# Optimization experiments

Hardware: AMD Instinct MI355X
Metric: run time of the kernel (lower is better)

## Reference

```python
import jax, jax.numpy as jnp
import numpy as np

B, L, C, H, W = 4, 16, 64, 64, 64
F, NH, NB = 128, 2, 2


def _ln(x, w, b, eps=1e-5):
    # LayerNorm over last two dims (H, W), torch-style biased variance
    m = jnp.mean(x, axis=(-2, -1), keepdims=True)
    v = jnp.var(x, axis=(-2, -1), keepdims=True)
    return (x - m) * jax.lax.rsqrt(v + eps) * w + b


def _conv2d(x, w, b):
    # x: (N, Cin, H, W), w: (Cout, Cin, k, k) -- the (1,k,k) Conv3d acts per-frame
    y = jax.lax.conv_general_dilated(x, w, (1, 1), 'SAME',
                                     dimension_numbers=('NCHW', 'OIHW', 'NCHW'))
    return y + b[None, :, None, None]


def _combine(c1, c2):
    a1, b1 = c1
    a2, b2 = c2
    return a1 * a2, a2 * b1 + b2


def _forward(x, params_log, pBw_r, pBw_i, pBb_r, pBb_i, pCw_r, pCw_i, pCb_r, pCb_i,
             lru_ln_w, lru_ln_b, cin_w, cin_b, h3_w, h3_b, h1_w, h1_b,
             h_ln_w, h_ln_b, cout_w, cout_b, ffn_ln_w, ffn_ln_b):
    gelu = lambda t: jax.nn.gelu(t, approximate=False)
    Bsz, Ln, Cc, Hh, Ww = x.shape
    for i in range(NB):
        # ---- ConvLRULayer ----
        pl = params_log[i]
        nu = jnp.exp(pl[:Cc])            # (C, H)
        theta = jnp.exp(pl[Cc:2 * Cc])   # (C, H)
        gamma = jnp.exp(pl[2 * Cc:])     # (C, H)
        lamb = jnp.exp(jax.lax.complex(-nu, theta))  # (C, H) complex
        Bw = jax.lax.complex(pBw_r[i], pBw_i[i])
        Bb = jax.lax.complex(pBb_r[i], pBb_i[i])
        Cw = jax.lax.complex(pCw_r[i], pCw_i[i])
        Cb = jax.lax.complex(pCb_r[i], pCb_i[i])
        h = jnp.fft.fft2(x.astype(jnp.complex64), axes=(-2, -1))  # (B,L,C,H,W)
        h = jnp.einsum('blchw,oc->blohw', h, Bw) + Bb[None, None, :, None, None]
        h = h * gamma[None, None, :, :, None]
        # parallel scan: h[t] = lamb * h[t-1] + h[t] along L
        a = jnp.broadcast_to(lamb[None, None, :, :, None], (Bsz, Ln, Cc, Hh, 1))
        _, h = jax.lax.associative_scan(_combine, (a, h), axis=1)
        h = jnp.fft.ifft2(h, axes=(-2, -1))
        h = jnp.einsum('blchw,oc->blohw', h, Cw) + Cb[None, None, :, None, None]
        h = _ln(h.real, lru_ln_w[i], lru_ln_b[i])
        x = h + x
        # ---- FeedForward (all Conv3d have kernel 1 in L -> per-frame 2D) ----
        y = x.reshape(Bsz * Ln, Cc, Hh, Ww)
        y_ = gelu(_conv2d(y, cin_w[i], cin_b[i]))  # (B*L, F, H, W)
        for j in range(NH):
            t = gelu(_conv2d(y_, h3_w[i, j], h3_b[i, j]))
            t = gelu(jnp.einsum('nfhw,of->nohw', t, h1_w[i, j])
                     + h1_b[i, j][None, :, None, None])
            y_ = _ln(t, h_ln_w[i, j], h_ln_b[i, j]) + y_
        t = jnp.einsum('nfhw,of->nohw', y_, cout_w[i]) + cout_b[i][None, :, None, None]
        t = _ln(t, ffn_ln_w[i], ffn_ln_b[i])
        x = t.reshape(Bsz, Ln, Cc, Hh, Ww) + x
    return x


def setup_inputs() -> dict:
    key = jax.random.key(0)
    ks = jax.random.split(key, 16)
    x = jax.random.normal(ks[0], (B, L, C, H, W), jnp.float32)
    # LRU stability init (as in the torch module)
    r_min, r_max = 0.8, 0.99
    u1 = jax.random.uniform(ks[1], (NB, C, H), jnp.float32)
    u2 = jax.random.uniform(ks[2], (NB, C, H), jnp.float32)
    nu_log = jnp.log(-0.5 * jnp.log(u1 * (r_max ** 2 - r_min ** 2) + r_min ** 2))
    theta_log = jnp.log(u2 * 2.0 * np.pi)
    gamma_log = 0.5 * jnp.log(1.0 - jnp.exp(-2.0 * jnp.exp(nu_log)))
    params_log = jnp.concatenate([nu_log, theta_log, gamma_log], axis=1)  # (NB, 3C, H)

    def nrm(k, shape, fan_in):
        return jax.random.normal(k, shape, jnp.float32) / np.sqrt(fan_in)

    return dict(
        x=x, params_log=params_log,
        pBw_r=nrm(ks[3], (NB, C, C), C), pBw_i=jnp.zeros((NB, C, C), jnp.float32),
        pBb_r=jnp.zeros((NB, C), jnp.float32), pBb_i=jnp.zeros((NB, C), jnp.float32),
        pCw_r=nrm(ks[4], (NB, C, C), C), pCw_i=jnp.zeros((NB, C, C), jnp.float32),
        pCb_r=jnp.zeros((NB, C), jnp.float32), pCb_i=jnp.zeros((NB, C), jnp.float32),
        lru_ln_w=jnp.ones((NB, H, W), jnp.float32), lru_ln_b=jnp.zeros((NB, H, W), jnp.float32),
        cin_w=nrm(ks[5], (NB, F, C, 7, 7), C * 49), cin_b=jnp.zeros((NB, F), jnp.float32),
        h3_w=nrm(ks[6], (NB, NH, F, F, 3, 3), F * 9), h3_b=jnp.zeros((NB, NH, F), jnp.float32),
        h1_w=nrm(ks[7], (NB, NH, F, F), F), h1_b=jnp.zeros((NB, NH, F), jnp.float32),
        h_ln_w=jnp.ones((NB, NH, H, W), jnp.float32), h_ln_b=jnp.zeros((NB, NH, H, W), jnp.float32),
        cout_w=nrm(ks[8], (NB, C, F), F), cout_b=jnp.zeros((NB, C), jnp.float32),
        ffn_ln_w=jnp.ones((NB, H, W), jnp.float32), ffn_ln_b=jnp.zeros((NB, H, W), jnp.float32),
    )


def reference(x, params_log, pBw_r, pBw_i, pBb_r, pBb_i, pCw_r, pCw_i, pCb_r, pCb_i,
              lru_ln_w, lru_ln_b, cin_w, cin_b, h3_w, h3_b, h1_w, h1_b,
              h_ln_w, h_ln_b, cout_w, cout_b, ffn_ln_w, ffn_ln_b):
    return _forward(x, params_log, pBw_r, pBw_i, pBb_r, pBb_i, pCw_r, pCw_i,
                    pCb_r, pCb_i, lru_ln_w, lru_ln_b, cin_w, cin_b, h3_w, h3_b,
                    h1_w, h1_b, h_ln_w, h_ln_b, cout_w, cout_b, ffn_ln_w, ffn_ln_b)
```

## Files before the change

### kernel.cpp

```cpp
#include <hip/hip_runtime.h>
#include <math.h>

static constexpr int Bd = 4, Ld = 16, Cd = 64, Hd = 64, Wd = 64, Fd = 128;
static constexpr int NBLK = 2, NHEAD = 2;
static constexpr int HW = 4096;
static constexpr float TWO_PI = 6.28318530717958647692f;

typedef __attribute__((ext_vector_type(8))) short bf16x8;
typedef __attribute__((ext_vector_type(4))) float f32x4;
typedef __attribute__((ext_vector_type(4))) unsigned int u32x4;

__device__ __forceinline__ float gelu_f(float v) {
    float x2 = v * v;
    float u = v * (0.797884560802865f + 0.0356774081363f * x2);
    float au = fabsf(u);
    float e = __expf(-2.f * au);
    float th = (1.f - e) * __builtin_amdgcn_rcpf(1.f + e);
    th = copysignf(th, u);
    return 0.5f * v * (1.f + th);
}

__device__ __forceinline__ unsigned short bf16c(float f) {
    unsigned int u = __float_as_uint(f);
    unsigned int r = (u + 0x7fffu + ((u >> 16) & 1u)) >> 16;
    return (unsigned short)r;
}
__device__ __forceinline__ float bf2f(unsigned short u) {
    return __uint_as_float((unsigned int)u << 16);
}
__device__ __forceinline__ unsigned int packbf(float r, float i) {
    return (unsigned int)bf16c(r) | ((unsigned int)bf16c(i) << 16);
}
__device__ __forceinline__ bf16x8 bneg(bf16x8 v) {
    u32x4 u = *(u32x4*)&v;
    u = u ^ 0x80008000u;
    return *(bf16x8*)&u;
}

__device__ __forceinline__ void gl2lds16(const void* g, void* l) {
    __builtin_amdgcn_global_load_lds(
        (const __attribute__((address_space(1))) void*)g,
        (__attribute__((address_space(3))) void*)l, 16, 0, 0);
}

__global__ void k_prepdft(unsigned short* __restrict__ o) {
    int idx = blockIdx.x * 256 + threadIdx.x;
    if (idx >= 16384) return;
    int sec = idx >> 12, j = idx & 4095;
    int a = j >> 6, b = j & 63;
    float ang = (TWO_PI / 64.f) * (float)((a * b) & 63);
    float sv, cv;
    __sincosf(ang, &sv, &cv);
    float v;
    if (sec == 0) v = cv;
    else if (sec == 1) v = -sv;
    else if (sec == 2) v = cv * (1.f / 64.f);
    else v = -sv * (1.f / 64.f);
    o[idx] = bf16c(v);
}

__global__ void k_preplru(const float* __restrict__ bwr, const float* __restrict__ bwi,
                          const float* __restrict__ cwr, const float* __restrict__ cwi,
                          const float* __restrict__ gl,
                          unsigned short* __restrict__ wout, float* __restrict__ gamT) {
    int idx = blockIdx.x * 256 + threadIdx.x;
    if (idx < 16384) {
        int sec = idx >> 12, j = idx & 4095;
        const float* s = (sec == 0) ? bwr : (sec == 1) ? bwi : (sec == 2) ? cwr : cwi;
        wout[idx] = bf16c(s[j]);
    } else if (idx < 20480) {
        int j = idx - 16384;
        int fh = j >> 6, o2 = j & 63;
        gamT[j] = __expf(gl[o2 * 64 + fh]);
    }
}

__global__ __launch_bounds__(256) void k_dfthm(const float* __restrict__ x,
                                               unsigned int* __restrict__ X,
                                               const unsigned short* __restrict__ tcb,
                                               const unsigned short* __restrict__ tsb) {
    __shared__ __align__(16) unsigned char smm[49152];
    unsigned char* xpT = smm;
    unsigned char* tC = smm + 32768;
    unsigned char* tS = smm + 40960;
    int blk = blockIdx.x;
    int fi = blk >> 4;
    int w0 = (blk & 15) * 4;
    int t = threadIdx.x, lane = t & 63, wv = t >> 6;
    int pl = lane & 15, kg = lane >> 4;
    int l3 = lane >> 3, l7 = lane & 7;

    for (int q = 0; q < 2; ++q) {
        int sg = q * 4 + wv;
        gl2lds16(tcb + (size_t)(sg * 8 + l3) * 64 + (l7 ^ l3) * 8, tC + sg * 1024);
        gl2lds16(tsb + (size_t)(sg * 8 + l3) * 64 + (l7 ^ l3) * 8, tS + sg * 1024);
    }
    const float* xf = x + (size_t)fi * Cd * HW;
    int h = t & 63;
    for (int k = 0; k < 16; ++k) {
        int c = k * 4 + (t >> 6);
        float4 v = *(const float4*)(xf + (size_t)c * HW + h * 64 + w0);
        float vv[4] = {v.x, v.y, v.z, v.w};
#pragma unroll
        for (int q = 0; q < 4; ++q) {
            int pos = q * 64 + c;
            *(unsigned short*)(xpT + pos * 128 + ((h * 2) ^ ((c & 7) << 4))) = bf16c(vv[q]);
        }
    }
    __syncthreads();

    int w = w0 + wv;
    unsigned int* Xw = X + (size_t)fi * 262144 + (size_t)w * 4096;
    for (int half = 0; half < 2; ++half) {
        f32x4 aR[2][4], aI[2][4];
#pragma unroll
        for (int mt = 0; mt < 2; ++mt)
#pragma unroll
            for (int nt = 0; nt < 4; ++nt) { aR[mt][nt] = (f32x4)0.f; aI[mt][nt] = (f32x4)0.f; }
#pragma unroll
        for (int ks = 0; ks < 2; ++ks) {
            int koff = (ks * 64 + kg * 16);
            bf16x8 ac[2], as_[2], b[4];
#pragma unroll
            for (int mt = 0; mt < 2; ++mt) {
                int row = half * 32 + mt * 16 + pl;
                int off = row * 128 + (koff ^ ((pl & 7) << 4));
                ac[mt] = *(const bf16x8*)(tC + off);
                as_[mt] = *(const bf16x8*)(tS + off);
            }
#pragma unroll
            for (int nt = 0; nt < 4; ++nt) {
                int pos = wv * 64 + nt * 16 + pl;
                b[nt] = *(const bf16x8*)(xpT + pos * 128 + (koff ^ ((pl & 7) << 4)));
            }
#pragma unroll
            for (int mt = 0; mt < 2; ++mt)
#pragma unroll
                for (int nt = 0; nt < 4; ++nt) {
                    aR[mt][nt] = __builtin_amdgcn_mfma_f32_16x16x32_bf16(ac[mt], b[nt], aR[mt][nt], 0, 0, 0);
                    aI[mt][nt] = __builtin_amdgcn_mfma_f32_16x16x32_bf16(as_[mt], b[nt], aI[mt][nt], 0, 0, 0);
                }
        }
#pragma unroll
        for (int mt = 0; mt < 2; ++mt)
#pragma unroll
            for (int nt = 0; nt < 4; ++nt) {
                int c = nt * 16 + pl;
#pragma unroll
                for (int r = 0; r < 4; ++r) {
                    int fh = half * 32 + mt * 16 + kg * 4 + r;
                    Xw[fh * 64 + c] = packbf(aR[mt][nt][r], aI[mt][nt][r]);
                }
            }
    }
}

__global__ __launch_bounds__(256) void k_lrumid(unsigned int* __restrict__ X,
                                                const unsigned short* __restrict__ wbr,
                                                const unsigned short* __restrict__ wbi,
                                                const unsigned short* __restrict__ wcr,
                                                const unsigned short* __restrict__ wci,
                                                const float* __restrict__ gamT,
                                                const float* __restrict__ br_g,
                                                const float* __restrict__ bi_g,
                                                const float* __restrict__ plg) {
    __shared__ __align__(16) unsigned char smm[81920];
    unsigned char* inr = smm;
    unsigned char* ini = smm + 8192;
    unsigned char* hre = smm + 16384;
    unsigned char* him = smm + 24576;
    unsigned char* wBR = smm + 32768;
    unsigned char* wBI = smm + 40960;
    unsigned char* wCR = smm + 49152;
    unsigned char* wCI = smm + 57344;
    float* gam = (float*)(smm + 65536);
    int blk = blockIdx.x;
    int b = blk >> 6, s = blk & 63;
    int t = threadIdx.x, lane = t & 63, wv = t >> 6;
    int pj = lane & 15, kg = lane >> 4;
    int l3 = lane >> 3, l7 = lane & 7;

    for (int q = 0; q < 2; ++q) {
        int sg = q * 4 + wv;
        size_t goff = (size_t)(sg * 8 + l3) * 64 + (l7 ^ l3) * 8;
        gl2lds16(wbr + goff, wBR + sg * 1024);
        gl2lds16(wbi + goff, wBI + sg * 1024);
        gl2lds16(wcr + goff, wCR + sg * 1024);
        gl2lds16(wci + goff, wCI + sg * 1024);
    }
    for (int j = t; j < 4096; j += 256) gam[j] = gamT[j];

    float lamr[4][4], lami[4][4];
#pragma unroll
    for (int nt = 0; nt < 4; ++nt) {
        int o = nt * 16 + pj;
#pragma unroll
        for (int r = 0; r < 4; ++r) {
            int fh = wv * 16 + kg * 4 + r;
            float nu = expf(plg[o * 64 + fh]);
            float th = expf(plg[4096 + o * 64 + fh]);
            float mag = expf(-nu);
            float sth, cth;
            sincosf(th, &sth, &cth);
            lamr[nt][r] = mag * cth;
            lami[nt][r] = mag * sth;
        }
    }
    float bRo[4], bIo[4];
#pragma unroll
    for (int nt = 0; nt < 4; ++nt) {
        bRo[nt] = (s == 0) ? br_g[nt * 16 + pj] : 0.f;
        bIo[nt] = (s == 0) ? bi_g[nt * 16 + pj] : 0.f;
    }
    float str[4][4], sti[4][4];
    unsigned int* Xfrm = X + (size_t)b * 16 * 262144 + (size_t)s * 4096;

    for (int l = 0; l < 16; ++l) {
        unsigned int* Xi = Xfrm + (size_t)l * 262144;
        __syncthreads();
        for (int k = 0; k < 4; ++k) {
            int j = k * 256 + t;
            int row = j >> 4, c0 = (j & 15) * 4;
            u32x4 v = *(const u32x4*)(Xi + (size_t)row * 64 + c0);
            unsigned int rw0 = (v.x & 0xffffu) | (v.y << 16);
            unsigned int rw1 = (v.z & 0xffffu) | (v.w << 16);
            unsigned int iw0 = (v.x >> 16) | (v.y & 0xffff0000u);
            unsigned int iw1 = (v.z >> 16) | (v.w & 0xffff0000u);
            int off = row * 128 + ((((c0 >> 3) ^ (row & 7)) << 4) | ((c0 & 7) * 2));
            *(unsigned int*)(inr + off) = rw0;
            *(unsigned int*)(inr + off + 4) = rw1;
            *(unsigned int*)(ini + off) = iw0;
            *(unsigned int*)(ini + off + 4) = iw1;
        }
        __syncthreads();

        f32x4 cR[4], cI[4];
#pragma unroll
        for (int nt = 0; nt < 4; ++nt) { cR[nt] = (f32x4)0.f; cI[nt] = (f32x4)0.f; }
#pragma unroll
        for (int ks = 0; ks < 2; ++ks) {
            int koff = ks * 64 + kg * 16;
            int aoff = (wv * 16 + pj) * 128 + (koff ^ ((pj & 7) << 4));
            bf16x8 ar = *(const bf16x8*)(inr + aoff);
            bf16x8 ai = *(const bf16x8*)(ini + aoff);
            bf16x8 an = bneg(ai);
#pragma unroll
            for (int nt = 0; nt < 4; ++nt) {
                int o = nt * 16 + pj;
                int woff = o * 128 + (koff ^ ((pj & 7) << 4));
                bf16x8 brf = *(const bf16x8*)(wBR + woff);
                bf16x8 bif = *(const bf16x8*)(wBI + woff);
                cR[nt] = __builtin_amdgcn_mfma_f32_16x16x32_bf16(ar, brf, cR[nt], 0, 0, 0);
                cR[nt] = __builtin_amdgcn_mfma_f32_16x16x32_bf16(an, bif, cR[nt], 0, 0, 0);
                cI[nt] = __builtin_amdgcn_mfma_f32_16x16x32_bf16(ar, bif, cI[nt], 0, 0, 0);
                cI[nt] = __builtin_amdgcn_mfma_f32_16x16x32_bf16(ai, brf, cI[nt], 0, 0, 0);
            }
        }
#pragma unroll
        for (int nt = 0; nt < 4; ++nt) {
            int o = nt * 16 + pj;
#pragma unroll
            for (int r = 0; r < 4; ++r) {
                int row = wv * 16 + kg * 4 + r;
                float g = gam[row * 64 + o];
                float vr = (cR[nt][r] + bRo[nt]) * g;
                float vi = (cI[nt][r] + bIo[nt]) * g;
                if (l == 0) {
                    str[nt][r] = vr;
                    sti[nt][r] = vi;
                } else {
                    float nr = lamr[nt][r] * str[nt][r] - lami[nt][r] * sti[nt][r] + vr;
                    float ni = lamr[nt][r] * sti[nt][r] + lami[nt][r] * str[nt][r] + vi;
                    str[nt][r] = nr;
                    sti[nt][r] = ni;
                }
                int hoff = row * 128 + ((((o >> 3) ^ (row & 7)) << 4) | ((o & 7) * 2));
                *(unsigned short*)(hre + hoff) = bf16c(str[nt][r]);
                *(unsigned short*)(him + hoff) = bf16c(sti[nt][r]);
            }
        }
        __syncthreads();

        f32x4 dR[4], dI[4];
#pragma unroll
        for (int nt = 0; nt < 4; ++nt) { dR[nt] = (f32x4)0.f; dI[nt] = (f32x4)0.f; }
#pragma unroll
        for (int ks = 0; ks < 2; ++ks) {
            int koff = ks * 64 + kg * 16;
            int aoff = (wv * 16 + pj) * 128 + (koff ^ ((pj & 7) << 4));
            bf16x8 ar = *(const bf16x8*)(hre + aoff);
            bf16x8 ai = *(const bf16x8*)(him + aoff);
            bf16x8 an = bneg(ai);
#pragma unroll
            for (int nt = 0; nt < 4; ++nt) {
                int o = nt * 16 + pj;
                int woff = o * 128 + (koff ^ ((pj & 7) << 4));
                bf16x8 brf = *(const bf16x8*)(wCR + woff);
                bf16x8 bif = *(const bf16x8*)(wCI + woff);
                dR[nt] = __builtin_amdgcn_mfma_f32_16x16x32_bf16(ar, brf, dR[nt], 0, 0, 0);
                dR[nt] = __builtin_amdgcn_mfma_f32_16x16x32_bf16(an, bif, dR[nt], 0, 0, 0);
                dI[nt] = __builtin_amdgcn_mfma_f32_16x16x32_bf16(ar, bif, dI[nt], 0, 0, 0);
                dI[nt] = __builtin_amdgcn_mfma_f32_16x16x32_bf16(ai, brf, dI[nt], 0, 0, 0);
            }
        }
#pragma unroll
        for (int nt = 0; nt < 4; ++nt) {
            int o = nt * 16 + pj;
#pragma unroll
            for (int r = 0; r < 4; ++r) {
                int row = wv * 16 + kg * 4 + r;
                Xi[(size_t)row * 64 + o] = packbf(dR[nt][r], dI[nt][r]);
            }
        }
    }
}

__global__ __launch_bounds__(256) void k_idfthm_ln(const unsigned int* __restrict__ X,
                                                   const unsigned short* __restrict__ tic,
                                                   const unsigned short* __restrict__ tis,
                                                   const float* __restrict__ cbr,
                                                   const float* __restrict__ lnw,
                                                   const float* __restrict__ lnb,
                                                   const float* __restrict__ xprev,
                                                   float* __restrict__ xout) {
    __shared__ __align__(16) unsigned char smm[81920];
    unsigned char* SrT = smm;
    unsigned char* SiT = smm + 32768;
    unsigned char* tC = smm + 65536;
    unsigned char* tS = smm + 73728;
    float* y4 = (float*)smm;
    int blk = blockIdx.x;
    int fi = blk >> 4;
    int c0 = (blk & 15) * 4;
    int t = threadIdx.x, lane = t & 63, wv = t >> 6;
    int pl = lane & 15, kg = lane >> 4;
    int l3 = lane >> 3, l7 = lane & 7;

    for (int q = 0; q < 2; ++q) {
        int sg = q * 4 + wv;
        gl2lds16(tic + (size_t)(sg * 8 + l3) * 64 + (l7 ^ l3) * 8, tC + sg * 1024);
        gl2lds16(tis + (size_t)(sg * 8 + l3) * 64 + (l7 ^ l3) * 8, tS + sg * 1024);
    }
    const unsigned int* Xf = X + (size_t)fi * 262144;
    int fh = t & 63;
    for (int k = 0; k < 16; ++k) {
        int w = k * 4 + (t >> 6);
        u32x4 v = *(const u32x4*)(Xf + (size_t)w * 4096 + fh * 64 + c0);
        unsigned int vv[4] = {v.x, v.y, v.z, v.w};
#pragma unroll
        for (int cj = 0; cj < 4; ++cj) {
            int pos2 = w * 4 + cj;
            int off = pos2 * 128 + ((fh * 2) ^ ((pos2 & 7) << 4));
            *(unsigned short*)(SrT + off) = (unsigned short)(vv[cj] & 0xffffu);
            *(unsigned short*)(SiT + off) = (unsigned short)(vv[cj] >> 16);
        }
    }
    __syncthreads();

    f32x4 y[4][4];
#pragma unroll
    for (int mt = 0; mt < 4; ++mt)
#pragma unroll
        for (int nt = 0; nt < 4; ++nt) y[mt][nt] = (f32x4)0.f;
#pragma unroll
    for (int ks = 0; ks < 2; ++ks) {
        int koff = ks * 64 + kg * 16;
        bf16x8 ac[4], as_[4], brf[4], bif[4];
#pragma unroll
        for (int mt = 0; mt < 4; ++mt) {
            int row = mt * 16 + pl;
            int off = row * 128 + (koff ^ ((pl & 7) << 4));
            ac[mt] = *(const bf16x8*)(tC + off);
            as_[mt] = *(const bf16x8*)(tS + off);
        }
#pragma unroll
        for (int nt = 0; nt < 4; ++nt) {
            int pos2 = wv * 64 + nt * 16 + pl;
            int off = pos2 * 128 + (koff ^ ((pl & 7) << 4));
            brf[nt] = *(const bf16x8*)(SrT + off);
            bif[nt] = *(const bf16x8*)(SiT + off);
        }
#pragma unroll
        for (int mt = 0; mt < 4; ++mt)
#pragma unroll
            for (int nt = 0; nt < 4; ++nt) {
                y[mt][nt] = __builtin_amdgcn_mfma_f32_16x16x32_bf16(ac[mt], brf[nt], y[mt][nt], 0, 0, 0);
                y[mt][nt] = __builtin_amdgcn_mfma_f32_16x16x32_bf16(as_[mt], bif[nt], y[mt][nt], 0, 0, 0);
            }
    }
    __syncthreads();

    float cb4[4];
#pragma unroll
    for (int cj = 0; cj < 4; ++cj) cb4[cj] = cbr[c0 + cj];
#pragma unroll
    for (int mt = 0; mt < 4; ++mt)
#pragma unroll
        for (int nt = 0; nt < 4; ++nt) {
            int pos2 = wv * 64 + nt * 16 + pl;
            int w = pos2 >> 2, cj = pos2 & 3;
#pragma unroll
            for (int r = 0; r < 4; ++r) {
                int h = mt * 16 + kg * 4 + r;
                y4[cj * 4232 + h * 66 + w] = y[mt][nt][r] + cb4[cj];
            }
        }
    __syncthreads();

    int w = lane;
    const float* yp = y4 + wv * 4232;
    float s = 0.f, q = 0.f;
    for (int h = 0; h < 64; ++h) {
        float v = yp[h * 66 + w];
        s += v;
        q += v * v;
    }
#pragma unroll
    for (int off = 32; off; off >>= 1) {
        s += __shfl_xor(s, off);
        q += __shfl_xor(q, off);
    }
    float m = s * (1.f / 4096.f);
    float var = q * (1.f / 4096.f) - m * m;
    float rs = rsqrtf(var + 1e-5f);
    int c = c0 + wv;
    const float* xp = xprev + ((size_t)fi * Cd + c) * HW;
    float* xo = xout + ((size_t)fi * Cd + c) * HW;
    for (int h = 0; h < 64; ++h) {
        int p = h * 64 + w;
        xo[p] = (yp[h * 66 + w] - m) * rs * lnw[p] + lnb[p] + xp[p];
    }
}

__global__ __launch_bounds__(256) void k_ln_res(const unsigned short* __restrict__ t_in,
                                                const float* __restrict__ w,
                                                const float* __restrict__ b,
                                                float* __restrict__ dst) {
    __shared__ float red[8];
    int fr = blockIdx.x;
    int t = threadIdx.x;
    const unsigned short* src = t_in + (size_t)fr * HW + t * 16;
    float* d = dst + (size_t)fr * HW + t * 16;
    u32x4 v0 = *(const u32x4*)(src);
    u32x4 v1 = *(const u32x4*)(src + 8);
    float vals[16];
    unsigned int vw[8] = {v0.x, v0.y, v0.z, v0.w, v1.x, v1.y, v1.z, v1.w};
#pragma unroll
    for (int j = 0; j < 8; ++j) {
        vals[j * 2] = bf2f((unsigned short)(vw[j] & 0xffffu));
        vals[j * 2 + 1] = bf2f((unsigned short)(vw[j] >> 16));
    }
    float s = 0.f, sq = 0.f;
#pragma unroll
    for (int j = 0; j < 16; ++j) { s += vals[j]; sq += vals[j] * vals[j]; }
    for (int off = 32; off; off >>= 1) {
        s += __shfl_down(s, off);
        sq += __shfl_down(sq, off);
    }
    int wid = t >> 6;
    if ((t & 63) == 0) { red[wid] = s; red[4 + wid] = sq; }
    __syncthreads();
    s = red[0] + red[1] + red[2] + red[3];
    sq = red[4] + red[5] + red[6] + red[7];
    float m = s * (1.f / 4096.f);
    float var = sq * (1.f / 4096.f) - m * m;
    float rs = rsqrtf(var + 1e-5f);
    const float* wp = w + t * 16;
    const float* bp = b + t * 16;
#pragma unroll
    for (int q4 = 0; q4 < 4; ++q4) {
        float4 wv4 = *(const float4*)(wp + q4 * 4);
        float4 bv4 = *(const float4*)(bp + q4 * 4);
        float4 dv = *(const float4*)(d + q4 * 4);
        dv.x += (vals[q4 * 4 + 0] - m) * rs * wv4.x + bv4.x;
        dv.y += (vals[q4 * 4 + 1] - m) * rs * wv4.y + bv4.y;
        dv.z += (vals[q4 * 4 + 2] - m) * rs * wv4.z + bv4.z;
        dv.w += (vals[q4 * 4 + 3] - m) * rs * wv4.w + bv4.w;
        *(float4*)(d + q4 * 4) = dv;
    }
}

__global__ void k_prep7(const float* __restrict__ w, unsigned short* __restrict__ o) {
    int idx = blockIdx.x * 256 + threadIdx.x;
    if (idx < 49 * 128 * 64) {
        int tap = idx >> 13, rem = idx & 8191, f = rem >> 6, c = rem & 63;
        o[idx] = bf16c(w[(size_t)(f * 64 + c) * 49 + tap]);
    }
}
__global__ void k_prep3(const float* __restrict__ w, unsigned short* __restrict__ o,
                        int nh) {
    int idx = blockIdx.x * 256 + threadIdx.x;
    if (idx < nh * 147456) {
        int head = idx / 147456;
        int rem = idx - head * 147456;
        int tap = rem >> 14, r2 = rem & 16383, f = r2 >> 7, c = r2 & 127;
        o[idx] = bf16c(w[(size_t)head * 147456 + (size_t)(f * 128 + c) * 9 + tap]);
    }
}
__global__ void k_prepcvt(const float* __restrict__ w, unsigned short* __restrict__ o, int n) {
    int idx = blockIdx.x * 256 + threadIdx.x;
    if (idx < n) o[idx] = bf16c(w[idx]);
}

__global__ __launch_bounds__(256) void k_t2p(const float* __restrict__ x,
                                             unsigned short* __restrict__ xT) {
    __shared__ float tile[64][65];
    int blk = blockIdx.x;
    int f = blk >> 6;
    int p0 = (blk & 63) * 64;
    int t = threadIdx.x;
    const float* src = x + (size_t)f * Cd * HW;
    for (int j = t; j < 4096; j += 256) {
        int c = j >> 6, p = j & 63;
        tile[c][p] = src[(size_t)c * HW + p0 + p];
    }
    __syncthreads();
    unsigned short* dst = xT + ((size_t)f * HW + p0) * 64;
    for (int j = t; j < 4096; j += 256) {
        int p = j >> 6, c = j & 63;
        dst[(size_t)p * 64 + c] = bf16c(tile[c][p]);
    }
}

__global__ __launch_bounds__(512) void k_conv7m(const unsigned short* __restrict__ xT,
                                                const unsigned short* __restrict__ wb,
                                                const float* __restrict__ bias,
                                                unsigned short* __restrict__ yout) {
    __shared__ __align__(16) unsigned char smm[158208];
    unsigned char* inT = smm;
    unsigned char* wt0 = smm + 125440;
    int blk = blockIdx.x;
    int fi = blk >> 3;
    int y0 = (blk & 7) * 8;
    int t = threadIdx.x, lane = t & 63, wv = t >> 6;
    int l3 = lane >> 3, l7 = lane & 7;

    const unsigned short* xf = xT + (size_t)fi * HW * 64;
    float4 z4 = make_float4(0.f, 0.f, 0.f, 0.f);
    int ksw_in = l7 ^ ((3 + l3) & 7);
    for (int idx = wv; idx < 112; idx += 8) {
        int r = idx >> 3, sg = idx & 7;
        int srow = y0 + r - 3;
        unsigned char* dst = inT + r * 8960 + 3 * 128 + sg * 1024;
        if (srow >= 0 && srow < 64) {
            gl2lds16(xf + (size_t)srow * 4096 + (sg * 8 + l3) * 64 + ksw_in * 8, dst);
        } else {
            *(float4*)(dst + lane * 16) = z4;
        }
    }
    for (int j = t; j < 672; j += 512) {
        int r = j / 48, k = j % 48;
        int xp = (k < 24) ? (k >> 3) : 67 + ((k - 24) >> 3);
        *(float4*)(inT + r * 8960 + xp * 128 + (k & 7) * 16) = z4;
    }
    int ksw_w = l7 ^ l3;
    for (int q = 0; q < 2; ++q) {
        int sg = q * 8 + wv;
        int f = sg * 8 + l3;
        gl2lds16(wb + (size_t)f * 64 + ksw_w * 8, wt0 + sg * 1024);
    }
    __syncthreads();

    int wm = wv & 3, wn = wv >> 2;
    f32x4 acc[8][4];
#pragma unroll
    for (int m = 0; m < 8; ++m)
#pragma unroll
        for (int n = 0; n < 4; ++n) acc[m][n] = (f32x4)0.f;
    int kg = lane >> 4, pl = lane & 15;
    int cur = 0;
    for (int tap = 0; tap < 49; ++tap) {
        if (tap + 1 < 49) {
            const unsigned short* g = wb + (size_t)(tap + 1) * 8192;
            unsigned char* wdst = wt0 + (cur ^ 1) * 16384;
            for (int q = 0; q < 2; ++q) {
                int sg = q * 8 + wv;
                int f = sg * 8 + l3;
                gl2lds16(g + (size_t)f * 64 + ksw_w * 8, wdst + sg * 1024);
            }
        }
        unsigned char* wcur = wt0 + cur * 16384;
        int ky = tap / 7, kx = tap % 7;
#pragma unroll
        for (int ks = 0; ks < 2; ++ks) {
            bf16x8 a[8], b[4];
#pragma unroll
            for (int m = 0; m < 8; ++m) {
                int row = wm * 2 + (m >> 2) + ky;
                int xp = (m & 3) * 16 + pl + kx;
                a[m] = *(const bf16x8*)(inT + row * 8960 + xp * 128 +
                                        (((ks * 4 + kg) ^ (xp & 7)) << 4));
            }
#pragma unroll
            for (int n = 0; n < 4; ++n) {
                int rowf = wn * 64 + n * 16 + pl;
                b[n] = *(const bf16x8*)(wcur + rowf * 128 +
                                        (((ks * 4 + kg) ^ (pl & 7)) << 4));
            }
#pragma unroll
            for (int m = 0; m < 8; ++m)
#pragma unroll
                for (int n = 0; n < 4; ++n)
                    acc[m][n] = __builtin_amdgcn_mfma_f32_16x16x32_bf16(a[m], b[n], acc[m][n], 0, 0, 0);
        }
        __syncthreads();
        cur ^= 1;
    }
    unsigned short* yo = yout + ((size_t)fi * HW + (size_t)y0 * 64) * 128;
#pragma unroll
    for (int m = 0; m < 8; ++m) {
        int rowl = wm * 2 + (m >> 2);
#pragma unroll
        for (int n = 0; n < 4; ++n) {
            int f = wn * 64 + n * 16 + pl;
            float bs = bias[f];
#pragma unroll
            for (int r = 0; r < 4; ++r) {
                int x = (m & 3) * 16 + kg * 4 + r;
                yo[(size_t)(rowl * 64 + x) * 128 + f] = bf16c(gelu_f(acc[m][n][r] + bs));
            }
        }
    }
}

__global__ __launch_bounds__(512) void k_conv3f(const unsigned short* __restrict__ yin,
                                                const unsigned short* __restrict__ wb,
                                                const float* __restrict__ bias3,
                                                const unsigned short* __restrict__ w1,
                                                const float* __restrict__ bias1,
                                                unsigned short* __restrict__ outp2,
                                                float* __restrict__ lnpart) {
    __shared__ __align__(16) unsigned char smm[163840];
    unsigned char* inT = smm;
    unsigned char* wt0 = smm + 98304;
    int blk = blockIdx.x;
    int fi = blk >> 4;
    int y0 = (blk & 15) * 4;
    int t = threadIdx.x, lane = t & 63, wv = t >> 6;
    int l4 = lane >> 4, l15 = lane & 15;
    const unsigned short* yf = yin + (size_t)fi * HW * 128;
    float4 z4 = make_float4(0.f, 0.f, 0.f, 0.f);
    for (int seg = wv; seg < 96; seg += 8) {
        int r = seg >> 4, xs = seg & 15;
        int srow = y0 + r - 1;
        int col = xs * 4 + l4;
        unsigned char* dst = inT + r * 16384 + xs * 4 * 256;
        if (srow >= 0 && srow < 64) {
            int gs = l15 ^ (col & 7);
            gl2lds16(yf + ((size_t)(srow * 64 + col) * 128 + gs * 8), dst);
        } else {
            *(float4*)(dst + lane * 16) = z4;
        }
    }
    for (int q = 0; q < 4; ++q) {
        int sg = q * 8 + wv;
        int f = sg * 4 + l4;
        gl2lds16(wb + (size_t)f * 128 + (l15 ^ (f & 7)) * 8, wt0 + sg * 1024);
    }
    __syncthreads();

    int wm = wv & 3, wn = wv >> 2;
    f32x4 acc[4][4];
#pragma unroll
    for (int m = 0; m < 4; ++m)
#pragma unroll
        for (int n = 0; n < 4; ++n) acc[m][n] = (f32x4)0.f;
    int kg = lane >> 4, pl = lane & 15;
    bf16x8 z8 = (bf16x8)(short)0;
    int cur = 0;
#pragma unroll
    for (int tap = 0; tap < 9; ++tap) {
        if (tap + 1 < 9) {
            const unsigned short* g = wb + (size_t)(tap + 1) * 16384;
            unsigned char* wdst = wt0 + (cur ^ 1) * 32768;
            for (int q = 0; q < 4; ++q) {
                int sg = q * 8 + wv;
                int f = sg * 4 + l4;
                gl2lds16(g + (size_t)f * 128 + (l15 ^ (f & 7)) * 8, wdst + sg * 1024);
            }
        }
        unsigned char* wcur = wt0 + cur * 32768;
        const int ky = tap / 3, kx = tap % 3;
        int rbase = (wm + ky) * 16384;
#pragma unroll
        for (int ks = 0; ks < 4; ++ks) {
            bf16x8 a[4], b[4];
#pragma unroll
            for (int m = 0; m < 4; ++m) {
                int col = m * 16 + pl + kx - 1;
                int colc = col;
                if (kx == 0 && m == 0) colc = (col < 0) ? 0 : col;
                if (kx == 2 && m == 3) colc = (col > 63) ? 63 : col;
                a[m] = *(const bf16x8*)(inT + rbase + colc * 256 +
                                        ((ks * 64 + kg * 16) ^ ((colc & 7) << 4)));
                if (kx == 0 && m == 0) a[m] = (pl == 0) ? z8 : a[m];
                if (kx == 2 && m == 3) a[m] = (pl == 15) ? z8 : a[m];
            }
#pragma unroll
            for (int n = 0; n < 4; ++n) {
                int row = wn * 64 + n * 16 + pl;
                b[n] = *(const bf16x8*)(wcur + (size_t)row * 256 +
                                        ((ks * 64 + kg * 16) ^ ((pl & 7) << 4)));
            }
#pragma unroll
            for (int m = 0; m < 4; ++m)
#pragma unroll
                for (int n = 0; n < 4; ++n)
                    acc[m][n] = __builtin_amdgcn_mfma_f32_16x16x32_bf16(a[m], b[n], acc[m][n], 0, 0, 0);
        }
        __syncthreads();
        cur ^= 1;
    }

    unsigned char* tL = smm;
    unsigned char* w1L = smm + 65536;
    float (*redS)[64] = (float (*)[64])(smm + 155648);
    float (*redQ)[64] = (float (*)[64])(smm + 157696);
#pragma unroll
    for (int m = 0; m < 4; ++m)
#pragma unroll
        for (int n = 0; n < 4; ++n) {
            int f = wn * 64 + n * 16 + pl;
            float bs = bias3[f];
#pragma unroll
            for (int r = 0; r < 4; ++r) {
                int pos = wm * 64 + m * 16 + kg * 4 + r;
                *(unsigned short*)(tL + (size_t)pos * 256 +
                    ((((f >> 3) ^ (pos & 7)) << 4) | ((f & 7) * 2))) =
                    bf16c(gelu_f(acc[m][n][r] + bs));
            }
        }
    for (int sg = wv; sg < 32; sg += 8) {
        int rr = sg * 4 + l4;
        gl2lds16(w1 + (size_t)rr * 128 + (l15 ^ (rr & 7)) * 8, w1L + sg * 1024);
    }
    __syncthreads();

    f32x4 fa[4][4];
#pragma unroll
    for (int m = 0; m < 4; ++m)
#pragma unroll
        for (int n = 0; n < 4; ++n) fa[m][n] = (f32x4)0.f;
#pragma unroll
    for (int ks = 0; ks < 4; ++ks) {
        bf16x8 a[4], b[4];
#pragma unroll
        for (int m = 0; m < 4; ++m) {
            int row = wm * 64 + m * 16 + pl;
            a[m] = *(const bf16x8*)(tL + (size_t)row * 256 +
                                    ((ks * 64 + kg * 16) ^ ((pl & 7) << 4)));
        }
#pragma unroll
        for (int n = 0; n < 4; ++n) {
            int row = wn * 64 + n * 16 + pl;
            b[n] = *(const bf16x8*)(w1L + (size_t)row * 256 +
                                    ((ks * 64 + kg * 16) ^ ((pl & 7) << 4)));
        }
#pragma unroll
        for (int m = 0; m < 4; ++m)
#pragma unroll
            for (int n = 0; n < 4; ++n)
                fa[m][n] = __builtin_amdgcn_mfma_f32_16x16x32_bf16(a[m], b[n], fa[m][n], 0, 0, 0);
    }
    __syncthreads();

    int slab = blk & 15;
    int p0 = slab * 256;
    unsigned char* oL = smm;
#pragma unroll
    for (int n = 0; n < 4; ++n) {
        int f = wn * 64 + n * 16 + pl;
        float bs = bias1[f];
        float s = 0.f, q = 0.f;
#pragma unroll
        for (int m = 0; m < 4; ++m)
#pragma unroll
            for (int r = 0; r < 4; ++r) {
                float v = gelu_f(fa[m][n][r] + bs);
                int pos = wm * 64 + m * 16 + kg * 4 + r;
                *(unsigned short*)(oL + (size_t)pos * 256 +
                    ((((f >> 3) ^ (pos & 7)) << 4) | ((f & 7) * 2))) = bf16c(v);
                s += v;
                q += v * v;
            }
        s += __shfl_xor(s, 16); s += __shfl_xor(s, 32);
        q += __shfl_xor(q, 16); q += __shfl_xor(q, 32);
        if (kg == 0) { redS[wv][n * 16 + pl] = s; redQ[wv][n * 16 + pl] = q; }
    }
    __syncthreads();
    unsigned char* o0 = (unsigned char*)(outp2 + ((size_t)fi * HW + p0) * 128);
#pragma unroll
    for (int it = 0; it < 8; ++it) {
        int gid = it * 512 + t;
        int pos = gid >> 4, g = gid & 15;
        u32x4 v = *(const u32x4*)(oL + (size_t)pos * 256 + ((g ^ (pos & 7)) << 4));
        *(u32x4*)(o0 + (size_t)pos * 256 + g * 16) = v;
    }
    if (t < 128) {
        int wh = t >> 6, j = t & 63;
        float s = redS[wh * 4][j] + redS[wh * 4 + 1][j] + redS[wh * 4 + 2][j] + redS[wh * 4 + 3][j];
        float q = redQ[wh * 4][j] + redQ[wh * 4 + 1][j] + redQ[wh * 4 + 2][j] + redQ[wh * 4 + 3][j];
        float* lp = lnpart + ((size_t)(fi * 16 + slab) * 128 + t) * 2;
        lp[0] = s;
        lp[1] = q;
    }
}

__global__ __launch_bounds__(256) void k_lnapply2(const unsigned short* __restrict__ t2,
                                                  const float* __restrict__ lnpart,
                                                  const float* __restrict__ w,
                                                  const float* __restrict__ b,
                                                  unsigned short* __restrict__ y) {
    __shared__ float sm_m[128], sm_r[128];
    int blk = blockIdx.x;
    int fi = blk >> 5, p0 = (blk & 31) * 128;
    int t = threadIdx.x;
    if (t < 128) {
        float s = 0.f, q = 0.f;
        for (int sl = 0; sl < 16; ++sl) {
            const float* lp = lnpart + ((size_t)(fi * 16 + sl) * 128 + t) * 2;
            s += lp[0];
            q += lp[1];
        }
        float m = s * (1.f / 4096.f);
        float var = q * (1.f / 4096.f) - m * m;
        sm_m[t] = m;
        sm_r[t] = rsqrtf(var + 1e-5f);
    }
    __syncthreads();
    int f0 = (t & 15) * 8, prow = t >> 4;
    float mm[8], rr[8];
#pragma unroll
    for (int j = 0; j < 8; ++j) { mm[j] = sm_m[f0 + j]; rr[j] = sm_r[f0 + j]; }
#pragma unroll
    for (int pass = 0; pass < 8; ++pass) {
        int p = p0 + pass * 16 + prow;
        size_t idx = ((size_t)fi * HW + p) * 128 + f0;
        u32x4 tv = *(const u32x4*)(t2 + idx);
        u32x4 yv = *(const u32x4*)(y + idx);
        float wp = w[p], bp = b[p];
        unsigned int tw[4] = {tv.x, tv.y, tv.z, tv.w};
        unsigned int yw[4] = {yv.x, yv.y, yv.z, yv.w};
        unsigned int ow[4];
#pragma unroll
        for (int q4 = 0; q4 < 4; ++q4) {
            float t0 = bf2f((unsigned short)(tw[q4] & 0xffffu));
            float t1 = bf2f((unsigned short)(tw[q4] >> 16));
            float y0 = bf2f((unsigned short)(yw[q4] & 0xffffu));
            float y1 = bf2f((unsigned short)(yw[q4] >> 16));
            float o0 = y0 + (t0 - mm[q4 * 2]) * rr[q4 * 2] * wp + bp;
            float o1 = y1 + (t1 - mm[q4 * 2 + 1]) * rr[q4 * 2 + 1] * wp + bp;
            ow[q4] = packbf(o0, o1);
        }
        u32x4 ov;
        ov.x = ow[0]; ov.y = ow[1]; ov.z = ow[2]; ov.w = ow[3];
        *(u32x4*)(y + idx) = ov;
    }
}

__global__ __launch_bounds__(256) void k_coutm(const unsigned short* __restrict__ yin,
                                               const unsigned short* __restrict__ wt,
                                               const float* __restrict__ bias,
                                               unsigned short* __restrict__ outp) {
    __shared__ __align__(16) unsigned char smm[49152];
    unsigned char* inL = smm;
    unsigned char* wL = smm + 32768;
    int blk = blockIdx.x;
    int fi = blk >> 5;
    int p0 = (blk & 31) * 128;
    int t = threadIdx.x, lane = t & 63, wv = t >> 6;
    int l4 = lane >> 4, l15 = lane & 15;
    for (int sg = wv; sg < 16; sg += 4) {
        int r = sg * 4 + l4;
        gl2lds16(wt + (size_t)r * 128 + (l15 ^ (r & 7)) * 8, wL + sg * 1024);
    }
    const unsigned short* yb = yin + (size_t)fi * HW * 128;
    for (int sg = wv; sg < 32; sg += 4) {
        int pos = sg * 4 + l4;
        gl2lds16(yb + ((size_t)(p0 + pos) * 128 + (l15 ^ (pos & 7)) * 8), inL + sg * 1024);
    }
    __syncthreads();
    int wm = wv & 1, wn = wv >> 1;
    f32x4 acc[2][4];
#pragma unroll
    for (int m = 0; m < 2; ++m)
#pragma unroll
        for (int n = 0; n < 4; ++n) acc[m][n] = (f32x4)0.f;
    int kg = lane >> 4, pl = lane & 15;
#pragma unroll
    for (int ks = 0; ks < 4; ++ks) {
        bf16x8 a[2], b[4];
#pragma unroll
        for (int m = 0; m < 2; ++m) {
            int row = wm * 32 + m * 16 + pl;
            a[m] = *(const bf16x8*)(wL + (size_t)row * 256 +
                                    ((ks * 64 + kg * 16) ^ ((pl & 7) << 4)));
        }
#pragma unroll
        for (int n = 0; n < 4; ++n) {
            int row = wn * 64 + n * 16 + pl;
            b[n] = *(const bf16x8*)(inL + (size_t)row * 256 +
                                    ((ks * 64 + kg * 16) ^ ((pl & 7) << 4)));
        }
#pragma unroll
        for (int m = 0; m < 2; ++m)
#pragma unroll
            for (int n = 0; n < 4; ++n)
                acc[m][n] = __builtin_amdgcn_mfma_f32_16x16x32_bf16(a[m], b[n], acc[m][n], 0, 0, 0);
    }
    __syncthreads();
    unsigned char* oL = smm;
#pragma unroll
    for (int m = 0; m < 2; ++m)
#pragma unroll
        for (int n = 0; n < 4; ++n) {
            int posl = wn * 64 + n * 16 + pl;
#pragma unroll
            for (int r = 0; r < 4; ++r) {
                int c = wm * 32 + m * 16 + kg * 4 + r;
                *(unsigned short*)(oL + (size_t)c * 256 +
                    ((((posl >> 3) ^ (c & 7)) << 4) | ((posl & 7) * 2))) =
                    bf16c(acc[m][n][r] + bias[c]);
            }
        }
    __syncthreads();
#pragma unroll
    for (int it = 0; it < 4; ++it) {
        int gid = it * 256 + t;
        int c = gid >> 4, g = gid & 15;
        u32x4 v = *(const u32x4*)(oL + (size_t)c * 256 + ((g ^ (c & 7)) << 4));
        *(u32x4*)((unsigned char*)(outp + ((size_t)fi * 64 + c) * HW + p0) + g * 16) = v;
    }
}

extern "C" void kernel_launch(void* const* d_in, const int* in_sizes, int n_in,
                              void* d_out, int out_size, void* d_ws, size_t ws_size,
                              hipStream_t stream) {
    (void)in_sizes; (void)n_in; (void)out_size;
    const float* x_in  = (const float*)d_in[0];
    const float* pl    = (const float*)d_in[1];
    const float* pBw_r = (const float*)d_in[2];
    const float* pBw_i = (const float*)d_in[3];
    const float* pBb_r = (const float*)d_in[4];
    const float* pBb_i = (const float*)d_in[5];
    const float* pCw_r = (const float*)d_in[6];
    const float* pCw_i = (const float*)d_in[7];
    const float* pCb_r = (const float*)d_in[8];
    const float* pCb_i = (const float*)d_in[9];
    const float* lruw  = (const float*)d_in[10];
    const float* lrub  = (const float*)d_in[11];
    const float* cinw  = (const float*)d_in[12];
    const float* cinb  = (const float*)d_in[13];
    const float* h3w   = (const float*)d_in[14];
    const float* h3b   = (const float*)d_in[15];
    const float* h1w   = (const float*)d_in[16];
    const float* h1b   = (const float*)d_in[17];
    const float* hlnw  = (const float*)d_in[18];
    const float* hlnb  = (const float*)d_in[19];
    const float* coutw = (const float*)d_in[20];
    const float* coutb = (const float*)d_in[21];
    const float* flnw  = (const float*)d_in[22];
    const float* flnb  = (const float*)d_in[23];
    float* out = (float*)d_out;

    int FR = 8, LB = 1;
    {
        const int frs[6] = {64, 32, 16, 16, 8, 8};
        const int lbs[6] = {4, 4, 4, 2, 2, 1};
        for (int k = 0; k < 6; ++k) {
            size_t region = (size_t)lbs[k] * 16777216ULL;
            size_t ffn = (size_t)frs[k] * 3145728ULL;
            if (ffn > region) region = ffn;
            size_t needb = region + 1605632ULL + (size_t)frs[k] * 32768ULL + 65536ULL;
            if (needb <= ws_size) { FR = frs[k]; LB = lbs[k]; break; }
        }
    }
    size_t region = (size_t)LB * 16777216ULL;
    {
        size_t ffn = (size_t)FR * 3145728ULL;
        if (ffn > region) region = ffn;
    }
    unsigned char* ws = (unsigned char*)d_ws;
    unsigned int* Xb = (unsigned int*)ws;
    unsigned short* ybuf = (unsigned short*)ws;
    unsigned short* t2bf = (unsigned short*)(ws + (size_t)FR * 1048576);
    unsigned short* xT   = (unsigned short*)(ws + (size_t)FR * 2097152);
    unsigned short* cobuf = (unsigned short*)(ws + (size_t)FR * 2621440);
    unsigned char* wbase = ws + region;
    unsigned short* wb7  = (unsigned short*)(wbase);
    unsigned short* wb3  = (unsigned short*)(wbase + 802816);
    unsigned short* wb1  = (unsigned short*)(wbase + 1392640);
    unsigned short* wbco = (unsigned short*)(wbase + 1458176);
    unsigned short* dftT = (unsigned short*)(wbase + 1474560);
    unsigned short* lruW = (unsigned short*)(wbase + 1507328);
    float* gamT          = (float*)(wbase + 1540096);
    float* lnpart        = (float*)(wbase + 1556480);
    unsigned short* tcb = dftT;
    unsigned short* tsb = dftT + 4096;
    unsigned short* tic = dftT + 8192;
    unsigned short* tis = dftT + 12288;
    unsigned short* wBr = lruW;
    unsigned short* wBi = lruW + 4096;
    unsigned short* wCr = lruW + 8192;
    unsigned short* wCi = lruW + 12288;

    const int NCl = 4 / LB;
    const int NCf = 64 / FR;

    k_prepdft<<<64, 256, 0, stream>>>(dftT);

    for (int i = 0; i < NBLK; ++i) {
        const float* xsrc = (i == 0) ? x_in : out;

        k_preplru<<<80, 256, 0, stream>>>(pBw_r + (size_t)i * 4096,
                                          pBw_i + (size_t)i * 4096,
                                          pCw_r + (size_t)i * 4096,
                                          pCw_i + (size_t)i * 4096,
                                          pl + (size_t)i * 12288 + 8192, lruW, gamT);
        for (int cc = 0; cc < NCl; ++cc) {
            size_t boff = (size_t)cc * LB * 4194304;
            k_dfthm<<<LB * 256, 256, 0, stream>>>(xsrc + boff, Xb, tcb, tsb);
            k_lrumid<<<LB * 64, 256, 0, stream>>>(Xb, wBr, wBi, wCr, wCi, gamT,
                                                  pBb_r + (size_t)i * 64,
                                                  pBb_i + (size_t)i * 64,
                                                  pl + (size_t)i * 12288);
            k_idfthm_ln<<<LB * 256, 256, 0, stream>>>(Xb, tic, tis,
                                                      pCb_r + (size_t)i * 64,
                                                      lruw + (size_t)i * 4096,
                                                      lrub + (size_t)i * 4096,
                                                      xsrc + boff, out + boff);
        }

        k_prep7<<<1568, 256, 0, stream>>>(cinw + (size_t)i * 401408, wb7);
        k_prep3<<<1152, 256, 0, stream>>>(h3w + (size_t)i * 2 * 147456, wb3, 2);
        k_prepcvt<<<128, 256, 0, stream>>>(h1w + (size_t)i * 2 * 16384, wb1, 32768);
        k_prepcvt<<<32, 256, 0, stream>>>(coutw + (size_t)i * 8192, wbco, 8192);

        for (int cc = 0; cc < NCf; ++cc) {
            float* xb = out + (size_t)cc * FR * 262144;
            k_t2p<<<FR * 64, 256, 0, stream>>>(xb, xT);
            k_conv7m<<<FR * 8, 512, 0, stream>>>(xT, wb7, cinb + (size_t)i * 128, ybuf);
            for (int j = 0; j < NHEAD; ++j) {
                k_conv3f<<<FR * 16, 512, 0, stream>>>(ybuf, wb3 + (size_t)j * 147456,
                                                      h3b + (size_t)(i * 2 + j) * 128,
                                                      wb1 + (size_t)j * 16384,
                                                      h1b + (size_t)(i * 2 + j) * 128,
                                                      t2bf, lnpart);
                k_lnapply2<<<FR * 32, 256, 0, stream>>>(t2bf, lnpart,
                                                        hlnw + (size_t)(i * 2 + j) * 4096,
                                                        hlnb + (size_t)(i * 2 + j) * 4096,
                                                        ybuf);
            }
            k_coutm<<<FR * 32, 256, 0, stream>>>(ybuf, wbco, coutb + (size_t)i * 64, cobuf);
            k_ln_res<<<FR * 64, 256, 0, stream>>>(cobuf, flnw + (size_t)i * 4096,
                                                  flnb + (size_t)i * 4096, xb);
        }
    }
}
```

Before: 1.601 ms.

## Double conv3 block tile to 8 rows and split channel reduction in halves

The fused 3x3+1x1 conv kernel now processes 8 output rows per block instead of 4, halving the grid and the partial LayerNorm slabs. To fit shared memory, the 128-channel input reduction is split into two 64-channel passes, with the input halo and per-tap weights reloaded for each half. Each wave now holds twice as many accumulators (8x4 MFMA tiles), which raises register pressure and can lower occupancy. The smaller grid may also leave compute units idle.

```diff
diff --git a/kernel.cpp b/kernel.cpp
--- a/kernel.cpp
+++ b/kernel.cpp
@@ -632,121 +632,141 @@
                                                 float* __restrict__ lnpart) {
     __shared__ __align__(16) unsigned char smm[163840];
     unsigned char* inT = smm;
-    unsigned char* wt0 = smm + 98304;
+    unsigned char* wt0 = smm + 81920;
     int blk = blockIdx.x;
-    int fi = blk >> 4;
-    int y0 = (blk & 15) * 4;
+    int fi = blk >> 3;
+    int y0 = (blk & 7) * 8;
     int t = threadIdx.x, lane = t & 63, wv = t >> 6;
-    int l4 = lane >> 4, l15 = lane & 15;
+    int l3 = lane >> 3, l7 = lane & 7;
+    int kg = lane >> 4, pl = lane & 15;
     const unsigned short* yf = yin + (size_t)fi * HW * 128;
     float4 z4 = make_float4(0.f, 0.f, 0.f, 0.f);
-    for (int seg = wv; seg < 96; seg += 8) {
-        int r = seg >> 4, xs = seg & 15;
+    int gsw = l7 ^ l3;
+
+    for (int seg = wv; seg < 80; seg += 8) {
+        int r = seg >> 3, cs = seg & 7;
         int srow = y0 + r - 1;
-        int col = xs * 4 + l4;
-        unsigned char* dst = inT + r * 16384 + xs * 4 * 256;
+        unsigned char* dst = inT + r * 8192 + cs * 1024;
         if (srow >= 0 && srow < 64) {
-            int gs = l15 ^ (col & 7);
-            gl2lds16(yf + ((size_t)(srow * 64 + col) * 128 + gs * 8), dst);
+            int col = cs * 8 + l3;
+            gl2lds16(yf + ((size_t)(srow * 64 + col) * 128 + gsw * 8), dst);
         } else {
             *(float4*)(dst + lane * 16) = z4;
         }
     }
-    for (int q = 0; q < 4; ++q) {
+    for (int q = 0; q < 2; ++q) {
         int sg = q * 8 + wv;
-        int f = sg * 4 + l4;
-        gl2lds16(wb + (size_t)f * 128 + (l15 ^ (f & 7)) * 8, wt0 + sg * 1024);
+        int f = sg * 8 + l3;
+        gl2lds16(wb + (size_t)f * 128 + gsw * 8, wt0 + sg * 1024);
     }
     __syncthreads();
 
     int wm = wv & 3, wn = wv >> 2;
-    f32x4 acc[4][4];
-#pragma unroll
-    for (int m = 0; m < 4; ++m)
+    f32x4 acc[8][4];
+#pragma unroll
+    for (int m = 0; m < 8; ++m)
 #pragma unroll
         for (int n = 0; n < 4; ++n) acc[m][n] = (f32x4)0.f;
-    int kg = lane >> 4, pl = lane & 15;
     bf16x8 z8 = (bf16x8)(short)0;
     int cur = 0;
-#pragma unroll
-    for (int tap = 0; tap < 9; ++tap) {
-        if (tap + 1 < 9) {
-            const unsigned short* g = wb + (size_t)(tap + 1) * 16384;
-            unsigned char* wdst = wt0 + (cur ^ 1) * 32768;
-            for (int q = 0; q < 4; ++q) {
-                int sg = q * 8 + wv;
-                int f = sg * 4 + l4;
-                gl2lds16(g + (size_t)f * 128 + (l15 ^ (f & 7)) * 8, wdst + sg * 1024);
-            }
-        }
-        unsigned char* wcur = wt0 + cur * 32768;
-        const int ky = tap / 3, kx = tap % 3;
-        int rbase = (wm + ky) * 16384;
-#pragma unroll
-        for (int ks = 0; ks < 4; ++ks) {
-            bf16x8 a[4], b[4];
-#pragma unroll
-            for (int m = 0; m < 4; ++m) {
-                int col = m * 16 + pl + kx - 1;
-                int colc = col;
-                if (kx == 0 && m == 0) colc = (col < 0) ? 0 : col;
-                if (kx == 2 && m == 3) colc = (col > 63) ? 63 : col;
-                a[m] = *(const bf16x8*)(inT + rbase + colc * 256 +
-                                        ((ks * 64 + kg * 16) ^ ((colc & 7) << 4)));
-                if (kx == 0 && m == 0) a[m] = (pl == 0) ? z8 : a[m];
-                if (kx == 2 && m == 3) a[m] = (pl == 15) ? z8 : a[m];
-            }
-#pragma unroll
-            for (int n = 0; n < 4; ++n) {
-                int row = wn * 64 + n * 16 + pl;
-                b[n] = *(const bf16x8*)(wcur + (size_t)row * 256 +
-                                        ((ks * 64 + kg * 16) ^ ((pl & 7) << 4)));
-            }
-#pragma unroll
-            for (int m = 0; m < 4; ++m)
-#pragma unroll
-                for (int n = 0; n < 4; ++n)
-                    acc[m][n] = __builtin_amdgcn_mfma_f32_16x16x32_bf16(a[m], b[n], acc[m][n], 0, 0, 0);
-        }
-        __syncthreads();
-        cur ^= 1;
+    for (int kk = 0; kk < 2; ++kk) {
+        if (kk == 1) {
+            for (int seg = wv; seg < 80; seg += 8) {
+                int r = seg >> 3, cs = seg & 7;
+                int srow = y0 + r - 1;
+                unsigned char* dst = inT + r * 8192 + cs * 1024;
+                if (srow >= 0 && srow < 64) {
+                    int col = cs * 8 + l3;
+                    gl2lds16(yf + ((size_t)(srow * 64 + col) * 128 + 64 + gsw * 8), dst);
+                } else {
+                    *(float4*)(dst + lane * 16) = z4;
+                }
+            }
+            __syncthreads();
+        }
+#pragma unroll
+        for (int tap = 0; tap < 9; ++tap) {
+            if (!(kk == 1 && tap == 8)) {
+                int tapn = (tap == 8) ? 0 : tap + 1;
+                int kkn = kk + ((tap == 8) ? 1 : 0);
+                const unsigned short* g = wb + (size_t)tapn * 16384 + (size_t)kkn * 64;
+                unsigned char* wdst = wt0 + (cur ^ 1) * 16384;
+                for (int q = 0; q < 2; ++q) {
+                    int sg = q * 8 + wv;
+                    int f = sg * 8 + l3;
+                    gl2lds16(g + (size_t)f * 128 + gsw * 8, wdst + sg * 1024);
+                }
+            }
+            unsigned char* wcur = wt0 + cur * 16384;
+            const int ky = tap / 3, kx = tap % 3;
+#pragma unroll
+            for (int ks = 0; ks < 2; ++ks) {
+                bf16x8 a[8], b[4];
+#pragma unroll
+                for (int m = 0; m < 8; ++m) {
+                    int row = wm * 2 + (m >> 2) + ky;
+                    int col = (m & 3) * 16 + pl + kx - 1;
+                    int colc = col;
+                    if (kx == 0 && (m & 3) == 0) colc = (col < 0) ? 0 : col;
+                    if (kx == 2 && (m & 3) == 3) colc = (col > 63) ? 63 : col;
+                    a[m] = *(const bf16x8*)(inT + row * 8192 + colc * 128 +
+                                            (((ks * 4 + kg) ^ (colc & 7)) << 4));
+                    if (kx == 0 && (m & 3) == 0) a[m] = (pl == 0) ? z8 : a[m];
+                    if (kx == 2 && (m & 3) == 3) a[m] = (pl == 15) ? z8 : a[m];
+                }
+#pragma unroll
+                for (int n = 0; n < 4; ++n) {
+                    int f = wn * 64 + n * 16 + pl;
+                    b[n] = *(const bf16x8*)(wcur + f * 128 +
+                                            (((ks * 4 + kg) ^ (f & 7)) << 4));
+                }
+#pragma unroll
+                for (int m = 0; m < 8; ++m)
+#pragma unroll
+                    for (int n = 0; n < 4; ++n)
+                        acc[m][n] = __builtin_amdgcn_mfma_f32_16x16x32_bf16(a[m], b[n], acc[m][n], 0, 0, 0);
+            }
+            __syncthreads();
+            cur ^= 1;
+        }
     }
 
     unsigned char* tL = smm;
-    unsigned char* w1L = smm + 65536;
-    float (*redS)[64] = (float (*)[64])(smm + 155648);
-    float (*redQ)[64] = (float (*)[64])(smm + 157696);
-#pragma unroll
-    for (int m = 0; m < 4; ++m)
+    unsigned char* w1L = smm + 131072;
+    int l4 = lane >> 4, l15 = lane & 15;
+#pragma unroll
+    for (int m = 0; m < 8; ++m) {
+        int rowl = wm * 2 + (m >> 2);
 #pragma unroll
         for (int n = 0; n < 4; ++n) {
             int f = wn * 64 + n * 16 + pl;
             float bs = bias3[f];
 #pragma unroll
             for (int r = 0; r < 4; ++r) {
-                int pos = wm * 64 + m * 16 + kg * 4 + r;
+                int pos = rowl * 64 + (m & 3) * 16 + kg * 4 + r;
                 *(unsigned short*)(tL + (size_t)pos * 256 +
                     ((((f >> 3) ^ (pos & 7)) << 4) | ((f & 7) * 2))) =
                     bf16c(gelu_f(acc[m][n][r] + bs));
             }
         }
+    }
     for (int sg = wv; sg < 32; sg += 8) {
         int rr = sg * 4 + l4;
         gl2lds16(w1 + (size_t)rr * 128 + (l15 ^ (rr & 7)) * 8, w1L + sg * 1024);
     }
     __syncthreads();
 
-    f32x4 fa[4][4];
-#pragma unroll
-    for (int m = 0; m < 4; ++m)
+    f32x4 fa[8][4];
+#pragma unroll
+    for (int m = 0; m < 8; ++m)
 #pragma unroll
         for (int n = 0; n < 4; ++n) fa[m][n] = (f32x4)0.f;
 #pragma unroll
     for (int ks = 0; ks < 4; ++ks) {
-        bf16x8 a[4], b[4];
-#pragma unroll
-        for (int m = 0; m < 4; ++m) {
-            int row = wm * 64 + m * 16 + pl;
+        bf16x8 a[8], b[4];
+#pragma unroll
+        for (int m = 0; m < 8; ++m) {
+            int row = wm * 128 + m * 16 + pl;
             a[m] = *(const bf16x8*)(tL + (size_t)row * 256 +
                                     ((ks * 64 + kg * 16) ^ ((pl & 7) << 4)));
         }
@@ -757,27 +777,29 @@
                                     ((ks * 64 + kg * 16) ^ ((pl & 7) << 4)));
         }
 #pragma unroll
-        for (int m = 0; m < 4; ++m)
+        for (int m = 0; m < 8; ++m)
 #pragma unroll
             for (int n = 0; n < 4; ++n)
                 fa[m][n] = __builtin_amdgcn_mfma_f32_16x16x32_bf16(a[m], b[n], fa[m][n], 0, 0, 0);
     }
     __syncthreads();
 
-    int slab = blk & 15;
-    int p0 = slab * 256;
+    int slab = blk & 7;
+    int p0 = slab * 512;
     unsigned char* oL = smm;
+    float (*redS)[64] = (float (*)[64])(smm + 131072);
+    float (*redQ)[64] = (float (*)[64])(smm + 133120);
 #pragma unroll
     for (int n = 0; n < 4; ++n) {
         int f = wn * 64 + n * 16 + pl;
         float bs = bias1[f];
         float s = 0.f, q = 0.f;
 #pragma unroll
-        for (int m = 0; m < 4; ++m)
+        for (int m = 0; m < 8; ++m)
 #pragma unroll
             for (int r = 0; r < 4; ++r) {
                 float v = gelu_f(fa[m][n][r] + bs);
-                int pos = wm * 64 + m * 16 + kg * 4 + r;
+                int pos = wm * 128 + m * 16 + kg * 4 + r;
                 *(unsigned short*)(oL + (size_t)pos * 256 +
                     ((((f >> 3) ^ (pos & 7)) << 4) | ((f & 7) * 2))) = bf16c(v);
                 s += v;
@@ -790,7 +812,7 @@
     __syncthreads();
     unsigned char* o0 = (unsigned char*)(outp2 + ((size_t)fi * HW + p0) * 128);
 #pragma unroll
-    for (int it = 0; it < 8; ++it) {
+    for (int it = 0; it < 16; ++it) {
         int gid = it * 512 + t;
         int pos = gid >> 4, g = gid & 15;
         u32x4 v = *(const u32x4*)(oL + (size_t)pos * 256 + ((g ^ (pos & 7)) << 4));
@@ -800,7 +822,7 @@
         int wh = t >> 6, j = t & 63;
         float s = redS[wh * 4][j] + redS[wh * 4 + 1][j] + redS[wh * 4 + 2][j] + redS[wh * 4 + 3][j];
         float q = redQ[wh * 4][j] + redQ[wh * 4 + 1][j] + redQ[wh * 4 + 2][j] + redQ[wh * 4 + 3][j];
-        float* lp = lnpart + ((size_t)(fi * 16 + slab) * 128 + t) * 2;
+        float* lp = lnpart + ((size_t)(fi * 8 + slab) * 128 + t) * 2;
         lp[0] = s;
         lp[1] = q;
     }
@@ -817,8 +839,8 @@
     int t = threadIdx.x;
     if (t < 128) {
         float s = 0.f, q = 0.f;
-        for (int sl = 0; sl < 16; ++sl) {
-            const float* lp = lnpart + ((size_t)(fi * 16 + sl) * 128 + t) * 2;
+        for (int sl = 0; sl < 8; ++sl) {
+            const float* lp = lnpart + ((size_t)(fi * 8 + sl) * 128 + t) * 2;
             s += lp[0];
             q += lp[1];
         }
@@ -1041,11 +1063,11 @@
             k_t2p<<<FR * 64, 256, 0, stream>>>(xb, xT);
             k_conv7m<<<FR * 8, 512, 0, stream>>>(xT, wb7, cinb + (size_t)i * 128, ybuf);
             for (int j = 0; j < NHEAD; ++j) {
-                k_conv3f<<<FR * 16, 512, 0, stream>>>(ybuf, wb3 + (size_t)j * 147456,
-                                                      h3b + (size_t)(i * 2 + j) * 128,
-                                                      wb1 + (size_t)j * 16384,
-                                                      h1b + (size_t)(i * 2 + j) * 128,
-                                                      t2bf, lnpart);
+                k_conv3f<<<FR * 8, 512, 0, stream>>>(ybuf, wb3 + (size_t)j * 147456,
+                                                     h3b + (size_t)(i * 2 + j) * 128,
+                                                     wb1 + (size_t)j * 16384,
+                                                     h1b + (size_t)(i * 2 + j) * 128,
+                                                     t2bf, lnpart);
                 k_lnapply2<<<FR * 32, 256, 0, stream>>>(t2bf, lnpart,
                                                         hlnw + (size_t)(i * 2 + j) * 4096,
                                                         hlnb + (size_t)(i * 2 + j) * 4096,
```

New measurement: 1.715 ms. +7.1%, slower.
